# Kernel tuning notes

Hardware: AMD Instinct MI355X
Metric: run time of the kernel (lower is better)

Reference implementation:

```python
import jax, jax.numpy as jnp
import numpy as np

N = 50000   # nodes
E = 625000  # edges
H = 128     # hidden_size
G = 1000    # graphs
NUM_ATOM_FEATS = 9
ATOM_VOCAB = 119  # padded vocab for all 9 OGB atom feature tables


def gcn_conv(h, row, col, W, b, n_nodes):
    """PyG GCNConv with add_self_loops=True, symmetric normalization, edge_weight=None."""
    loop = jnp.arange(n_nodes)
    r = jnp.concatenate([row, loop])
    c = jnp.concatenate([col, loop])
    w = jnp.ones(r.shape[0], dtype=h.dtype)
    deg = jax.ops.segment_sum(w, c, num_segments=n_nodes)
    dinv = jnp.where(deg > 0, jax.lax.rsqrt(deg), 0.0)
    norm = dinv[r] * dinv[c]              # [E+N]
    hw = h @ W                            # [N, H] linear transform first
    msg = norm[:, None] * hw[r]           # gather + scale
    out = jax.ops.segment_sum(msg, c, num_segments=n_nodes)  # scatter-add
    return out + b


def setup_inputs() -> dict:
    key = jax.random.key(0)
    ks = jax.random.split(key, 12)
    s = 1.0 / np.sqrt(H)
    return {
        "x": jax.random.randint(ks[0], (N, NUM_ATOM_FEATS), 0, 2),
        "edge_index": jax.random.randint(ks[1], (2, E), 0, N),
        "batch": jnp.sort(jax.random.randint(ks[2], (N,), 0, G)),
        "emb": jax.random.normal(ks[3], (NUM_ATOM_FEATS, ATOM_VOCAB, H), dtype=jnp.float32) * 0.1,
        "W1": jax.random.normal(ks[4], (H, H), dtype=jnp.float32) * s,
        "b1": jnp.zeros((H,), dtype=jnp.float32),
        "W2": jax.random.normal(ks[5], (H, H), dtype=jnp.float32) * s,
        "b2": jnp.zeros((H,), dtype=jnp.float32),
        "W3": jax.random.normal(ks[6], (H, H), dtype=jnp.float32) * s,
        "b3": jnp.zeros((H,), dtype=jnp.float32),
        "lin_w": jax.random.normal(ks[7], (H, 1), dtype=jnp.float32) * s,
        "lin_b": jnp.zeros((1,), dtype=jnp.float32),
    }


def reference(x, edge_index, batch, emb, W1, b1, W2, b2, W3, b3, lin_w, lin_b):
    row, col = edge_index[0], edge_index[1]
    # AtomEncoder: sum of per-feature embeddings -> [N, H]
    h = emb[jnp.arange(NUM_ATOM_FEATS)[None, :], x].sum(axis=1)
    h = jax.nn.relu(gcn_conv(h, row, col, W1, b1, N))
    h = jax.nn.relu(gcn_conv(h, row, col, W2, b2, N))
    h = gcn_conv(h, row, col, W3, b3, N)
    # dropout(p=0.2) is identity in eval mode
    # global_mean_pool over graph ids
    sums = jax.ops.segment_sum(h, batch, num_segments=G)
    cnts = jax.ops.segment_sum(jnp.ones((N,), dtype=h.dtype), batch, num_segments=G)
    pooled = sums / jnp.clip(cnts, 1.0)[:, None]
    return jax.nn.sigmoid(pooled @ lin_w + lin_b)  # [G, 1]
```

## Files before the change

### kernel.cpp

```cpp
#include <hip/hip_runtime.h>
#include <hip/hip_bf16.h>
#include <math.h>

#define N_NODES 50000
#define N_EDGES 625000
#define HID 128
#define N_GRAPHS 1000
#define N_FEATS 9
#define VOCAB 119
#define SENTINEL N_NODES
#define CAP 64
#define CAPLOG 6
#define NPART 8
#define PARTSZ (N_NODES / NPART)
#define NB_SCAN ((N_NODES + 255) / 256)
#define LDSW 136
#define NBLK (N_NODES / 16)

#define FSLICE ((N_EDGES + 255) / 256)
#define FB (FSLICE * NPART)
#define PB ((32897 + N_NODES + 1 + 255) / 256)

typedef __attribute__((ext_vector_type(8))) short short8;
typedef __attribute__((ext_vector_type(8))) unsigned short ushort8;
typedef __attribute__((ext_vector_type(4))) float f32x4;

static __device__ __forceinline__ float bflo(unsigned int w) {
    return __uint_as_float(w << 16);
}
static __device__ __forceinline__ float bfhi(unsigned int w) {
    return __uint_as_float(w & 0xffff0000u);
}
static __device__ __forceinline__ unsigned int f2bf(float f) {
    unsigned int u = __float_as_uint(f);
    return (u + 0x7fffu + ((u >> 16) & 1u)) >> 16;
}
static __device__ __forceinline__ uint2 pack4(float a, float b, float c, float d) {
    uint2 r;
    r.x = f2bf(a) | (f2bf(b) << 16);
    r.y = f2bf(c) | (f2bf(d) << 16);
    return r;
}

__global__ __launch_bounds__(256) void init_k(int* __restrict__ cursor,
                                              unsigned int* __restrict__ hpA_sent,
                                              unsigned int* __restrict__ hpB_sent,
                                              float* __restrict__ sp) {
    int i = blockIdx.x * 256 + threadIdx.x;
    if (i < N_NODES) cursor[i] = 0;
    if (i < 64) { hpA_sent[i] = 0; hpB_sent[i] = 0; }
    if (i == 64) sp[SENTINEL] = 0.f;
}

__global__ __launch_bounds__(256) void mid_k(const int* __restrict__ row,
                                             const int* __restrict__ col,
                                             int* __restrict__ cursor,
                                             unsigned short* __restrict__ csrc,
                                             const float* __restrict__ W1,
                                             const float* __restrict__ W2,
                                             const float* __restrict__ W3,
                                             const float* __restrict__ b3,
                                             const float* __restrict__ lw,
                                             const int* __restrict__ batch,
                                             unsigned short* __restrict__ Wt,
                                             float* __restrict__ wtil,
                                             float* __restrict__ cbuf,
                                             int* __restrict__ goff) {
    int b = blockIdx.x;
    if (b < FB) {
        int slice = b >> 3;
        int part = b & 7;
        int e = slice * 256 + threadIdx.x;
        if (e >= N_EDGES) return;
        int c = col[e];
        if ((unsigned)(c - part * PARTSZ) < (unsigned)PARTSZ) {
            int pos = atomicAdd(&cursor[c], 1);
            if (pos < CAP)
                csrc[((size_t)c << CAPLOG) + pos] = (unsigned short)row[e];
        }
    } else {
        int t = (b - FB) * 256 + threadIdx.x;
        if (t < 32768) {
            int which = t >> 14;
            int rem = t & 16383;
            int n = rem >> 7, k = rem & 127;
            const float* W = which ? W2 : W1;
            Wt[which * 16384 + n * 128 + k] = (unsigned short)f2bf(W[k * 128 + n]);
        } else if (t < 32896) {
            int k = t - 32768;
            float s = 0.f;
            for (int n = 0; n < 128; n++) s += W3[k * 128 + n] * lw[n];
            wtil[k] = s;
        } else if (t == 32896) {
            float s = 0.f;
            for (int n = 0; n < 128; n++) s += b3[n] * lw[n];
            cbuf[0] = s;
        } else {
            int i = t - 32897;
            if (i > N_NODES) return;
            int bprev = (i == 0) ? -1 : batch[i - 1];
            int bcur = (i == N_NODES) ? N_GRAPHS : batch[i];
            for (int g = bprev + 1; g <= bcur; g++) goff[g] = i;
        }
    }
}

__global__ __launch_bounds__(256) void atomdinv_k(const int* __restrict__ x,
                                                  const float* __restrict__ emb,
                                                  const int* __restrict__ cursor,
                                                  float* __restrict__ dinv,
                                                  unsigned short* __restrict__ csrc,
                                                  unsigned short* __restrict__ hp) {
    int gid = blockIdx.x * 256 + threadIdx.x;
    int node = gid >> 5;
    int sub = gid & 31;
    if (node >= N_NODES) return;
    int d = cursor[node];
    float di = rsqrtf((float)(d + 1));
    if (sub == 0) {
        dinv[node] = di;
        if (d > CAP) d = CAP;
        int r8 = (d + 7) & ~7;
        if (r8 > CAP) r8 = CAP;
        unsigned short* bk = csrc + ((size_t)node << CAPLOG);
        for (int j = d; j < r8; j++) bk[j] = (unsigned short)SENTINEL;
    }
    int d4 = sub * 4;
    float4 acc = make_float4(0.f, 0.f, 0.f, 0.f);
#pragma unroll
    for (int f = 0; f < N_FEATS; f++) {
        int idx = x[node * N_FEATS + f];
        const float4 v = *(const float4*)(emb + ((size_t)(f * VOCAB + idx)) * HID + d4);
        acc.x += v.x; acc.y += v.y; acc.z += v.z; acc.w += v.w;
    }
    ((uint2*)hp)[(size_t)node * 32 + sub] =
        pack4(di * acc.x, di * acc.y, di * acc.z, di * acc.w);
}

template <int DOT>
__global__ __launch_bounds__(256) void fused_k(const unsigned short* __restrict__ hp_in,
                                               const unsigned short* __restrict__ Wt,
                                               const float* __restrict__ bias,
                                               const float* __restrict__ dinv,
                                               const int* __restrict__ deg,
                                               const unsigned short* __restrict__ csrc,
                                               unsigned short* __restrict__ hp_out,
                                               const float* __restrict__ wtil,
                                               float* __restrict__ sp) {
    __shared__ unsigned short a_sh[16 * LDSW];
    __shared__ float spart[64];
    int tid = threadIdx.x;
    int sub = tid & 15, nl = tid >> 4;
    int node = blockIdx.x * 16 + nl;
    const uint4* H = (const uint4*)hp_in;
    {
        int d = deg[node];
        if (d > CAP) d = CAP;
        int e = (d + 7) & ~7;
        if (e > CAP) e = CAP;
        const unsigned short* bk = csrc + ((size_t)node << CAPLOG);
        uint4 v = H[(size_t)node * 16 + sub];
        float a0 = bflo(v.x), a1 = bfhi(v.x), a2 = bflo(v.y), a3 = bfhi(v.y);
        float a4 = bflo(v.z), a5 = bfhi(v.z), a6 = bflo(v.w), a7 = bfhi(v.w);
        for (int i = 0; i < e; i += 8) {
            ushort8 r = *(const ushort8*)(bk + i);
            uint4 u0 = H[(size_t)r[0] * 16 + sub];
            uint4 u1 = H[(size_t)r[1] * 16 + sub];
            uint4 u2 = H[(size_t)r[2] * 16 + sub];
            uint4 u3 = H[(size_t)r[3] * 16 + sub];
            uint4 u4 = H[(size_t)r[4] * 16 + sub];
            uint4 u5 = H[(size_t)r[5] * 16 + sub];
            uint4 u6 = H[(size_t)r[6] * 16 + sub];
            uint4 u7 = H[(size_t)r[7] * 16 + sub];
            a0 += bflo(u0.x); a1 += bfhi(u0.x); a2 += bflo(u0.y); a3 += bfhi(u0.y);
            a4 += bflo(u0.z); a5 += bfhi(u0.z); a6 += bflo(u0.w); a7 += bfhi(u0.w);
            a0 += bflo(u1.x); a1 += bfhi(u1.x); a2 += bflo(u1.y); a3 += bfhi(u1.y);
            a4 += bflo(u1.z); a5 += bfhi(u1.z); a6 += bflo(u1.w); a7 += bfhi(u1.w);
            a0 += bflo(u2.x); a1 += bfhi(u2.x); a2 += bflo(u2.y); a3 += bfhi(u2.y);
            a4 += bflo(u2.z); a5 += bfhi(u2.z); a6 += bflo(u2.w); a7 += bfhi(u2.w);
            a0 += bflo(u3.x); a1 += bfhi(u3.x); a2 += bflo(u3.y); a3 += bfhi(u3.y);
            a4 += bflo(u3.z); a5 += bfhi(u3.z); a6 += bflo(u3.w); a7 += bfhi(u3.w);
            a0 += bflo(u4.x); a1 += bfhi(u4.x); a2 += bflo(u4.y); a3 += bfhi(u4.y);
            a4 += bflo(u4.z); a5 += bfhi(u4.z); a6 += bflo(u4.w); a7 += bfhi(u4.w);
            a0 += bflo(u5.x); a1 += bfhi(u5.x); a2 += bflo(u5.y); a3 += bfhi(u5.y);
            a4 += bflo(u5.z); a5 += bfhi(u5.z); a6 += bflo(u5.w); a7 += bfhi(u5.w);
            a0 += bflo(u6.x); a1 += bfhi(u6.x); a2 += bflo(u6.y); a3 += bfhi(u6.y);
            a4 += bflo(u6.z); a5 += bfhi(u6.z); a6 += bflo(u6.w); a7 += bfhi(u6.w);
            a0 += bflo(u7.x); a1 += bfhi(u7.x); a2 += bflo(u7.y); a3 += bfhi(u7.y);
            a4 += bflo(u7.z); a5 += bfhi(u7.z); a6 += bflo(u7.w); a7 += bfhi(u7.w);
        }
        float di = dinv[node];
        uint2 p0 = pack4(di * a0, di * a1, di * a2, di * a3);
        uint2 p1 = pack4(di * a4, di * a5, di * a6, di * a7);
        uint4 o; o.x = p0.x; o.y = p0.y; o.z = p1.x; o.w = p1.y;
        *(uint4*)(a_sh + nl * LDSW + sub * 8) = o;
    }
    __syncthreads();
    int w = tid >> 6, l = tid & 63;
    int lm = l & 15, lk = l >> 4;
    int cbase = w * 32;
    f32x4 acc[2];
    acc[0] = (f32x4)0.f; acc[1] = (f32x4)0.f;
#pragma unroll
    for (int kk = 0; kk < 4; kk++) {
        short8 af = *(const short8*)(a_sh + lm * LDSW + (kk * 4 + lk) * 8);
#pragma unroll
        for (int nt = 0; nt < 2; nt++) {
            short8 bf = *(const short8*)(Wt + (size_t)(cbase + nt * 16 + lm) * HID + (kk * 4 + lk) * 8);
            acc[nt] = __builtin_amdgcn_mfma_f32_16x16x32_bf16(bf, af, acc[nt], 0, 0, 0);
        }
    }
    int m = blockIdx.x * 16 + lm;
    float di = dinv[m];
    if (DOT == 0) {
#pragma unroll
        for (int nt = 0; nt < 2; nt++) {
            int n0 = cbase + nt * 16 + lk * 4;
            float4 b4 = *(const float4*)(bias + n0);
            float o0 = di * fmaxf(acc[nt][0] + b4.x, 0.f);
            float o1 = di * fmaxf(acc[nt][1] + b4.y, 0.f);
            float o2 = di * fmaxf(acc[nt][2] + b4.z, 0.f);
            float o3 = di * fmaxf(acc[nt][3] + b4.w, 0.f);
            *(uint2*)(hp_out + (size_t)m * HID + n0) = pack4(o0, o1, o2, o3);
        }
    } else {
        float s = 0.f;
#pragma unroll
        for (int nt = 0; nt < 2; nt++) {
            int n0 = cbase + nt * 16 + lk * 4;
            float4 b4 = *(const float4*)(bias + n0);
            float4 w4 = *(const float4*)(wtil + n0);
            s += di * fmaxf(acc[nt][0] + b4.x, 0.f) * w4.x
               + di * fmaxf(acc[nt][1] + b4.y, 0.f) * w4.y
               + di * fmaxf(acc[nt][2] + b4.z, 0.f) * w4.z
               + di * fmaxf(acc[nt][3] + b4.w, 0.f) * w4.w;
        }
        s += __shfl_xor(s, 16, 64);
        s += __shfl_xor(s, 32, 64);
        if (lk == 0) spart[w * 16 + lm] = s;
        __syncthreads();
        if (tid < 16)
            sp[blockIdx.x * 16 + tid] =
                spart[tid] + spart[16 + tid] + spart[32 + tid] + spart[48 + tid];
    }
}

__global__ __launch_bounds__(256) void gout_k(const float* __restrict__ sp,
                                              const int* __restrict__ goff,
                                              const int* __restrict__ deg,
                                              const unsigned short* __restrict__ csrc,
                                              const float* __restrict__ dinv,
                                              const float* __restrict__ cbuf,
                                              const float* __restrict__ lin_b,
                                              float* __restrict__ out) {
    int wave = (blockIdx.x * 256 + threadIdx.x) >> 6;
    int lane = threadIdx.x & 63;
    if (wave >= N_GRAPHS) return;
    int s0 = goff[wave], s1 = goff[wave + 1];
    float s = 0.f;
    for (int j = s0 + lane; j < s1; j += 64) {
        int d = deg[j];
        if (d > CAP) d = CAP;
        int ee = (d + 7) & ~7;
        if (ee > CAP) ee = CAP;
        const unsigned short* bk = csrc + ((size_t)j << CAPLOG);
        float acc = sp[j];
        for (int i = 0; i < ee; i += 4) {
            ushort4 r = *(const ushort4*)(bk + i);
            acc += sp[r.x] + sp[r.y] + sp[r.z] + sp[r.w];
        }
        s += dinv[j] * acc;
    }
#pragma unroll
    for (int o = 32; o >= 1; o >>= 1) s += __shfl_xor(s, o, 64);
    if (lane == 0) {
        int cnt = s1 - s0;
        float z = (cnt == 0) ? lin_b[0] : (s / (float)cnt + cbuf[0] + lin_b[0]);
        out[wave] = 1.0f / (1.0f + expf(-z));
    }
}

extern "C" void kernel_launch(void* const* d_in, const int* in_sizes, int n_in,
                              void* d_out, int out_size, void* d_ws, size_t ws_size,
                              hipStream_t stream) {
    const int* x      = (const int*)d_in[0];
    const int* ei     = (const int*)d_in[1];
    const int* batch  = (const int*)d_in[2];
    const float* emb  = (const float*)d_in[3];
    const float* W1   = (const float*)d_in[4];
    const float* b1   = (const float*)d_in[5];
    const float* W2   = (const float*)d_in[6];
    const float* b2   = (const float*)d_in[7];
    const float* W3   = (const float*)d_in[8];
    const float* b3   = (const float*)d_in[9];
    const float* lw   = (const float*)d_in[10];
    const float* lb   = (const float*)d_in[11];
    float* out = (float*)d_out;

    char* ws = (char*)d_ws;
    size_t off = 0;
    auto alloc = [&](size_t bytes) {
        void* p = ws + off;
        off = (off + bytes + 255) & ~(size_t)255;
        return p;
    };
    int*   cursor  = (int*)alloc((size_t)N_NODES * 4);
    float* dinv    = (float*)alloc((size_t)N_NODES * 4);
    unsigned short* csrc = (unsigned short*)alloc((size_t)N_NODES * CAP * 2);
    unsigned short* hpA  = (unsigned short*)alloc((size_t)(N_NODES + 1) * HID * 2);
    unsigned short* hpB  = (unsigned short*)alloc((size_t)(N_NODES + 1) * HID * 2);
    unsigned short* Wt   = (unsigned short*)alloc((size_t)2 * HID * HID * 2);
    float* wtil    = (float*)alloc((size_t)HID * 4);
    float* cbuf    = (float*)alloc(256);
    float* sp      = (float*)alloc((size_t)(N_NODES + 1) * 4);
    int*   goff    = (int*)alloc((size_t)(N_GRAPHS + 1) * 4);

    const int* row = ei;
    const int* col = ei + N_EDGES;

    init_k<<<NB_SCAN, 256, 0, stream>>>(cursor,
                                        (unsigned int*)(hpA + (size_t)SENTINEL * HID),
                                        (unsigned int*)(hpB + (size_t)SENTINEL * HID),
                                        sp);
    mid_k<<<FB + PB, 256, 0, stream>>>(row, col, cursor, csrc,
                                       W1, W2, W3, b3, lw, batch,
                                       Wt, wtil, cbuf, goff);
    atomdinv_k<<<(N_NODES * 32) / 256, 256, 0, stream>>>(x, emb, cursor, dinv, csrc, hpA);

    fused_k<0><<<NBLK, 256, 0, stream>>>(hpA, Wt, b1, dinv, cursor, csrc, hpB, wtil, sp);
    fused_k<1><<<NBLK, 256, 0, stream>>>(hpB, Wt + 16384, b2, dinv, cursor, csrc, hpA, wtil, sp);

    gout_k<<<(N_GRAPHS * 64 + 255) / 256, 256, 0, stream>>>(sp, goff, cursor, csrc,
                                                            dinv, cbuf, lb, out);
}
```

Measured before the change: 126.8 us.

## Move atom embedding into mid kernel and pad neighbor lists to four

The atom-embedding sum, which does not depend on degrees, now runs as extra blocks inside the edge-bucketing kernel and writes an unscaled bf16 copy into hpB. A lighter scale kernel then applies dinv and writes the sentinel padding. Neighbor lists are padded to multiples of 4 instead of 8, and the aggregation loops gain a 4-wide tail, so fewer sentinel rows are gathered. The cost is one extra bf16 round trip through memory and double rounding of the initial features to bf16.

```diff
diff --git a/kernel.cpp b/kernel.cpp
--- a/kernel.cpp
+++ b/kernel.cpp
@@ -20,6 +20,7 @@
 #define FSLICE ((N_EDGES + 255) / 256)
 #define FB (FSLICE * NPART)
 #define PB ((32897 + N_NODES + 1 + 255) / 256)
+#define AB ((N_NODES * 32) / 256)
 
 typedef __attribute__((ext_vector_type(8))) short short8;
 typedef __attribute__((ext_vector_type(8))) unsigned short ushort8;
@@ -65,7 +66,10 @@
                                              unsigned short* __restrict__ Wt,
                                              float* __restrict__ wtil,
                                              float* __restrict__ cbuf,
-                                             int* __restrict__ goff) {
+                                             int* __restrict__ goff,
+                                             const int* __restrict__ x,
+                                             const float* __restrict__ emb,
+                                             unsigned short* __restrict__ h0buf) {
     int b = blockIdx.x;
     if (b < FB) {
         int slice = b >> 3;
@@ -78,7 +82,7 @@
             if (pos < CAP)
                 csrc[((size_t)c << CAPLOG) + pos] = (unsigned short)row[e];
         }
-    } else {
+    } else if (b < FB + PB) {
         int t = (b - FB) * 256 + threadIdx.x;
         if (t < 32768) {
             int which = t >> 14;
@@ -102,15 +106,28 @@
             int bcur = (i == N_NODES) ? N_GRAPHS : batch[i];
             for (int g = bprev + 1; g <= bcur; g++) goff[g] = i;
         }
-    }
-}
-
-__global__ __launch_bounds__(256) void atomdinv_k(const int* __restrict__ x,
-                                                  const float* __restrict__ emb,
-                                                  const int* __restrict__ cursor,
-                                                  float* __restrict__ dinv,
-                                                  unsigned short* __restrict__ csrc,
-                                                  unsigned short* __restrict__ hp) {
+    } else {
+        int gid = (b - FB - PB) * 256 + threadIdx.x;
+        int node = gid >> 5;
+        int sub = gid & 31;
+        if (node >= N_NODES) return;
+        int d4 = sub * 4;
+        float4 acc = make_float4(0.f, 0.f, 0.f, 0.f);
+#pragma unroll
+        for (int f = 0; f < N_FEATS; f++) {
+            int idx = x[node * N_FEATS + f];
+            const float4 v = *(const float4*)(emb + ((size_t)(f * VOCAB + idx)) * HID + d4);
+            acc.x += v.x; acc.y += v.y; acc.z += v.z; acc.w += v.w;
+        }
+        ((uint2*)h0buf)[(size_t)node * 32 + sub] = pack4(acc.x, acc.y, acc.z, acc.w);
+    }
+}
+
+__global__ __launch_bounds__(256) void scale_k(const unsigned short* __restrict__ h0buf,
+                                               const int* __restrict__ cursor,
+                                               float* __restrict__ dinv,
+                                               unsigned short* __restrict__ csrc,
+                                               unsigned short* __restrict__ hp) {
     int gid = blockIdx.x * 256 + threadIdx.x;
     int node = gid >> 5;
     int sub = gid & 31;
@@ -120,21 +137,14 @@
     if (sub == 0) {
         dinv[node] = di;
         if (d > CAP) d = CAP;
-        int r8 = (d + 7) & ~7;
-        if (r8 > CAP) r8 = CAP;
+        int r4 = (d + 3) & ~3;
+        if (r4 > CAP) r4 = CAP;
         unsigned short* bk = csrc + ((size_t)node << CAPLOG);
-        for (int j = d; j < r8; j++) bk[j] = (unsigned short)SENTINEL;
-    }
-    int d4 = sub * 4;
-    float4 acc = make_float4(0.f, 0.f, 0.f, 0.f);
-#pragma unroll
-    for (int f = 0; f < N_FEATS; f++) {
-        int idx = x[node * N_FEATS + f];
-        const float4 v = *(const float4*)(emb + ((size_t)(f * VOCAB + idx)) * HID + d4);
-        acc.x += v.x; acc.y += v.y; acc.z += v.z; acc.w += v.w;
-    }
+        for (int j = d; j < r4; j++) bk[j] = (unsigned short)SENTINEL;
+    }
+    uint2 v = ((const uint2*)h0buf)[(size_t)node * 32 + sub];
     ((uint2*)hp)[(size_t)node * 32 + sub] =
-        pack4(di * acc.x, di * acc.y, di * acc.z, di * acc.w);
+        pack4(di * bflo(v.x), di * bfhi(v.x), di * bflo(v.y), di * bfhi(v.y));
 }
 
 template <int DOT>
@@ -156,13 +166,14 @@
     {
         int d = deg[node];
         if (d > CAP) d = CAP;
-        int e = (d + 7) & ~7;
-        if (e > CAP) e = CAP;
+        int r4 = (d + 3) & ~3;
+        if (r4 > CAP) r4 = CAP;
         const unsigned short* bk = csrc + ((size_t)node << CAPLOG);
         uint4 v = H[(size_t)node * 16 + sub];
         float a0 = bflo(v.x), a1 = bfhi(v.x), a2 = bflo(v.y), a3 = bfhi(v.y);
         float a4 = bflo(v.z), a5 = bfhi(v.z), a6 = bflo(v.w), a7 = bfhi(v.w);
-        for (int i = 0; i < e; i += 8) {
+        int i = 0;
+        for (; i + 8 <= r4; i += 8) {
             ushort8 r = *(const ushort8*)(bk + i);
             uint4 u0 = H[(size_t)r[0] * 16 + sub];
             uint4 u1 = H[(size_t)r[1] * 16 + sub];
@@ -189,6 +200,21 @@
             a0 += bflo(u7.x); a1 += bfhi(u7.x); a2 += bflo(u7.y); a3 += bfhi(u7.y);
             a4 += bflo(u7.z); a5 += bfhi(u7.z); a6 += bflo(u7.w); a7 += bfhi(u7.w);
         }
+        if (i < r4) {
+            ushort4 r = *(const ushort4*)(bk + i);
+            uint4 u0 = H[(size_t)r.x * 16 + sub];
+            uint4 u1 = H[(size_t)r.y * 16 + sub];
+            uint4 u2 = H[(size_t)r.z * 16 + sub];
+            uint4 u3 = H[(size_t)r.w * 16 + sub];
+            a0 += bflo(u0.x); a1 += bfhi(u0.x); a2 += bflo(u0.y); a3 += bfhi(u0.y);
+            a4 += bflo(u0.z); a5 += bfhi(u0.z); a6 += bflo(u0.w); a7 += bfhi(u0.w);
+            a0 += bflo(u1.x); a1 += bfhi(u1.x); a2 += bflo(u1.y); a3 += bfhi(u1.y);
+            a4 += bflo(u1.z); a5 += bfhi(u1.z); a6 += bflo(u1.w); a7 += bfhi(u1.w);
+            a0 += bflo(u2.x); a1 += bfhi(u2.x); a2 += bflo(u2.y); a3 += bfhi(u2.y);
+            a4 += bflo(u2.z); a5 += bfhi(u2.z); a6 += bflo(u2.w); a7 += bfhi(u2.w);
+            a0 += bflo(u3.x); a1 += bfhi(u3.x); a2 += bflo(u3.y); a3 += bfhi(u3.y);
+            a4 += bflo(u3.z); a5 += bfhi(u3.z); a6 += bflo(u3.w); a7 += bfhi(u3.w);
+        }
         float di = dinv[node];
         uint2 p0 = pack4(di * a0, di * a1, di * a2, di * a3);
         uint2 p1 = pack4(di * a4, di * a5, di * a6, di * a7);
@@ -261,7 +287,7 @@
     for (int j = s0 + lane; j < s1; j += 64) {
         int d = deg[j];
         if (d > CAP) d = CAP;
-        int ee = (d + 7) & ~7;
+        int ee = (d + 3) & ~3;
         if (ee > CAP) ee = CAP;
         const unsigned short* bk = csrc + ((size_t)j << CAPLOG);
         float acc = sp[j];
@@ -322,10 +348,11 @@
                                         (unsigned int*)(hpA + (size_t)SENTINEL * HID),
                                         (unsigned int*)(hpB + (size_t)SENTINEL * HID),
                                         sp);
-    mid_k<<<FB + PB, 256, 0, stream>>>(row, col, cursor, csrc,
-                                       W1, W2, W3, b3, lw, batch,
-                                       Wt, wtil, cbuf, goff);
-    atomdinv_k<<<(N_NODES * 32) / 256, 256, 0, stream>>>(x, emb, cursor, dinv, csrc, hpA);
+    mid_k<<<FB + PB + AB, 256, 0, stream>>>(row, col, cursor, csrc,
+                                            W1, W2, W3, b3, lw, batch,
+                                            Wt, wtil, cbuf, goff,
+                                            x, emb, hpB);
+    scale_k<<<(N_NODES * 32) / 256, 256, 0, stream>>>(hpB, cursor, dinv, csrc, hpA);
 
     fused_k<0><<<NBLK, 256, 0, stream>>>(hpA, Wt, b1, dinv, cursor, csrc, hpB, wtil, sp);
     fused_k<1><<<NBLK, 256, 0, stream>>>(hpB, Wt + 16384, b2, dinv, cursor, csrc, hpA, wtil, sp);
```

New measurement: 134.0 us. 1.06x slower.
